# Performance work log

Hardware: AMD Instinct MI355X
Metric: run time of the kernel (lower is better)

Reference implementation:

```python
import jax, jax.numpy as jnp
import numpy as np
from jax import lax

S = 3000      # number of stocks (and number of targets)
F = 6         # raw features
N = 128       # hidden size
L = 40        # lookback length
L_MAX = 10    # max lag
K = 5         # topk leaders


def setup_inputs() -> dict:
    key = jax.random.key(0)
    ks = jax.random.split(key, 16)
    sc = 1.0 / np.sqrt(N)
    u = lambda k, shp, s=sc: jax.random.uniform(k, shp, jnp.float32, -s, s)
    return {
        "X_scaled": jax.random.normal(ks[0], (1, S, L, F), jnp.float32),
        "X_raw": jax.random.normal(ks[1], (1, S, L, F), jnp.float32),
        "target_idx": jax.random.randint(ks[2], (S,), 0, S, jnp.int32),
        "lstm_Wih": u(ks[3], (4 * N, F)),
        "lstm_Whh": u(ks[4], (4 * N, N)),
        "lstm_bih": u(ks[5], (4 * N,)),
        "lstm_bhh": u(ks[6], (4 * N,)),
        "ln_g": jnp.ones((N,), jnp.float32),
        "ln_b": jnp.zeros((N,), jnp.float32),
        "WQ": u(ks[7], (N, N)),
        "WK": u(ks[8], (N, N)),
        "log_temp": jnp.asarray(np.log(N ** 0.25), jnp.float32),
        "lag_bias": jnp.zeros((L_MAX,), jnp.float32),
        "W1": u(ks[9], (64, 2 * F), 1.0 / np.sqrt(2 * F)),
        "b1": jnp.zeros((64,), jnp.float32),
        "W2": u(ks[10], (32, 64), 1.0 / 8.0),
        "b2": jnp.zeros((32,), jnp.float32),
        "W3": u(ks[11], (1, 32), 1.0 / np.sqrt(32)),
        "b3": jnp.zeros((1,), jnp.float32),
    }


def _lstm(x, Wih, Whh, bih, bhh):
    # x: [BS, L, F] -> hidden sequence [BS, L, N]; torch gate order i,f,g,o
    BS = x.shape[0]
    h0 = jnp.zeros((BS, N), x.dtype)
    bias = bih + bhh

    def step(carry, xt):
        h, c = carry
        g = xt @ Wih.T + h @ Whh.T + bias
        i, f, gg, o = jnp.split(g, 4, axis=-1)
        c = jax.nn.sigmoid(f) * c + jax.nn.sigmoid(i) * jnp.tanh(gg)
        h = jax.nn.sigmoid(o) * jnp.tanh(c)
        return (h, c), h

    _, hs = lax.scan(step, (h0, h0), jnp.swapaxes(x, 0, 1))
    return jnp.swapaxes(hs, 0, 1)


def _ln(x, g, b):
    m = x.mean(-1, keepdims=True)
    v = ((x - m) ** 2).mean(-1, keepdims=True)
    return (x - m) / jnp.sqrt(v + 1e-5) * g + b


def _l2norm(x):
    return x / jnp.clip(jnp.linalg.norm(x, axis=-1, keepdims=True), 1e-12)


def reference(X_scaled, X_raw, target_idx, lstm_Wih, lstm_Whh, lstm_bih,
              lstm_bhh, ln_g, ln_b, WQ, WK, log_temp, lag_bias,
              W1, b1, W2, b2, W3, b3):
    # TemporalEncoder: LSTM over B*S sequences + LayerNorm (B=1)
    H = _ln(_lstm(X_scaled.reshape(S, L, F), lstm_Wih, lstm_Whh,
                  lstm_bih, lstm_bhh), ln_g, ln_b)          # [S, L, N]
    X = X_raw[0]                                            # [S, L, F]

    q = _l2norm(H[target_idx, -1] @ WQ.T)                   # [T, N]
    Hk = _l2norm(H[:, L - L_MAX:] @ WK.T)                   # [S, l_max, N]
    temp = jnp.clip(jnp.exp(log_temp), 0.1, N ** 0.5)

    attn = jnp.einsum('tn,sln->tsl', q, Hk) / temp + lag_bias  # [T, S, l_max]
    self_mask = jnp.arange(S)[None, :] == target_idx[:, None]  # [T, S]
    attn = jnp.where(self_mask[:, :, None], -jnp.inf, attn)

    vals, idx = lax.top_k(attn.reshape(-1, S * L_MAX), K)   # [T, K]
    leader = idx // L_MAX
    lag_j = idx % L_MAX
    lag_pos = jnp.clip(L - 1 - (L_MAX - lag_j), 0, L - 1)

    z = X[leader, lag_pos]                                  # [T, K, F]
    w = jax.nn.softmax(vals, axis=1)
    z_agg = (w[..., None] * z).sum(1)                       # [T, F]
    feat = jnp.concatenate([z_agg, z[:, 0]], axis=-1)       # [T, 2F]

    h1 = jax.nn.relu(feat @ W1.T + b1)
    h2 = jax.nn.relu(h1 @ W2.T + b2)
    return (h2 @ W3.T + b3).squeeze(-1)                     # [T]
```

## Files before the change

### kernel.cpp

```cpp
#include <hip/hip_runtime.h>
#include <math.h>

#define S_N 3000
#define NCOLS 30000
#define SCHUNK 8
#define KTILES 938
#define TPC 118
#define PST 17

typedef __bf16 v8bf __attribute__((ext_vector_type(8)));
typedef float v16f __attribute__((ext_vector_type(16)));
typedef float v4f __attribute__((ext_vector_type(4)));

__device__ __forceinline__ float sigm(float x) { return 1.0f / (1.0f + expf(-x)); }

__device__ __forceinline__ bool bet(float av, int ai, float bv, int bi) {
  return (av > bv) || (av == bv && ai < bi);
}

template <int M>
__device__ __forceinline__ void insS(float (&v)[M], int (&ix)[M], float nv, int ni) {
  if (!(nv > v[M - 1])) return;
  bool b[M];
#pragma unroll
  for (int q = 0; q < M; q++) b[q] = nv > v[q];
#pragma unroll
  for (int q = M - 1; q > 0; q--) {
    v[q]  = b[q] ? (b[q - 1] ? v[q - 1] : nv) : v[q];
    ix[q] = b[q] ? (b[q - 1] ? ix[q - 1] : ni) : ix[q];
  }
  if (b[0]) { v[0] = nv; ix[0] = ni; }
}

template <int M>
__device__ __forceinline__ void insF(float (&v)[M], int (&ix)[M], float nv, int ni) {
  if (!bet(nv, ni, v[M - 1], ix[M - 1])) return;
  bool b[M];
#pragma unroll
  for (int q = 0; q < M; q++) b[q] = bet(nv, ni, v[q], ix[q]);
#pragma unroll
  for (int q = M - 1; q > 0; q--) {
    v[q]  = b[q] ? (b[q - 1] ? v[q - 1] : nv) : v[q];
    ix[q] = b[q] ? (b[q - 1] ? ix[q - 1] : ni) : ix[q];
  }
  if (b[0]) { v[0] = nv; ix[0] = ni; }
}

__device__ __forceinline__ unsigned short f2bf_rne(float f) {
  unsigned int u = __float_as_uint(f);
  unsigned int r = (u + 0x7fffu + ((u >> 16) & 1u)) >> 16;
  return (unsigned short)r;
}
__device__ __forceinline__ float bf2f(unsigned short h) {
  return __uint_as_float(((unsigned int)h) << 16);
}

__global__ __launch_bounds__(256) void cvt_wll(
    const float* __restrict__ Whh, unsigned short* __restrict__ Wllf)
{
  int idx = blockIdx.x * 256 + threadIdx.x;
  if (idx >= 128 * 512) return;
  int f = idx >> 9;
  int lane = (idx >> 3) & 63;
  int j = idx & 7;
  int w = f >> 3, tau = (f >> 1) & 3, s = f & 1;
  int kh = w >> 3, g8 = w & 7;
  int gate = g8 * 64 + tau * 16 + (lane & 15);
  int k = kh * 64 + s * 32 + (lane >> 4) * 8 + j;
  float x = Whh[gate * 128 + k];
  unsigned short hi = f2bf_rne(x);
  float r1 = x - bf2f(hi);
  unsigned short lo = f2bf_rne(r1);
  float r2 = r1 - bf2f(lo);
  Wllf[idx] = f2bf_rne(r2);
}

__global__ __launch_bounds__(1024, 4) void lstm_kernel(
    const float* __restrict__ Xs, const float* __restrict__ Wih,
    const float* __restrict__ Whh, const float* __restrict__ bih,
    const float* __restrict__ bhh, const unsigned short* __restrict__ Wllf,
    float* __restrict__ H10)
{
  __shared__ float P[2 * 512 * PST];
  __shared__ __align__(16) __bf16 Asp[3][4][65][8];
  __shared__ float Xb[12 * 240];
  __shared__ float2 WB2[14][128];

  const int tid = threadIdx.x;
  const int s0 = blockIdx.x * 12;
  const int lane = tid & 63;
  const int wv = tid >> 6;
  const int kh = wv >> 3;
  const int g8 = wv & 7;
  const int l15 = lane & 15, lq = lane >> 4;

  for (int i = tid; i < 12 * 240; i += 1024) Xb[i] = Xs[(size_t)s0 * 240 + i];
  for (int i = tid; i < 3 * 4 * 65 * 8; i += 1024)
    ((unsigned short*)Asp)[i] = 0;
  for (int i = tid; i < 14 * 128; i += 1024) {
    int q = i >> 7, n = i & 127;
    float vv[2];
#pragma unroll
    for (int e = 0; e < 2; e++) {
      int r = 2 * q + e;
      if (r < 24) {
        int gate = n + (r / 6) * 128;
        vv[e] = Wih[gate * 6 + r % 6];
      } else {
        int gate = n + (r - 24) * 128;
        vv[e] = bih[gate] + bhh[gate];
      }
    }
    WB2[q][n] = make_float2(vv[0], vv[1]);
  }

  v8bf whi[4][2], wlo[4][2];
#pragma unroll
  for (int tau = 0; tau < 4; tau++)
#pragma unroll
    for (int s = 0; s < 2; s++) {
      int gate = g8 * 64 + tau * 16 + l15;
      int k0 = kh * 64 + s * 32 + lq * 8;
      const float* wp = Whh + gate * 128 + k0;
      v8bf h8, l8;
#pragma unroll
      for (int j = 0; j < 8; j++) {
        float x = wp[j];
        __bf16 bh_ = (__bf16)x;
        float r1 = x - (float)bh_;
        __bf16 bl_ = (__bf16)r1;
        h8[j] = bh_;
        l8[j] = bl_;
      }
      whi[tau][s] = h8;
      wlo[tau][s] = l8;
    }

  const unsigned short* wllbase = Wllf + (size_t)(wv * 8) * 512 + lane * 8;

  float c0 = 0.0f, c1 = 0.0f;
  const int p2n = tid & 127;
  const int p2m = tid >> 7;
  const int rdrow = (lane & 48) | ((lane + 2 * (lane >> 4)) & 15);

  __syncthreads();

#pragma unroll 1
  for (int t = 0; t < 40; t++) {
    v8bf ah[2], al[2], a3[2];
#pragma unroll
    for (int s = 0; s < 2; s++) {
      int ks = kh * 2 + s;
      ah[s] = *(const v8bf*)&Asp[0][ks][rdrow][0];
      al[s] = *(const v8bf*)&Asp[1][ks][rdrow][0];
      a3[s] = *(const v8bf*)&Asp[2][ks][rdrow][0];
    }
#pragma unroll
    for (int tau = 0; tau < 4; tau++) {
      v4f acc = {0.0f, 0.0f, 0.0f, 0.0f};
#pragma unroll
      for (int s = 0; s < 2; s++) {
        v8bf wll = *(const v8bf*)(wllbase + (tau * 2 + s) * 512);
        acc = __builtin_amdgcn_mfma_f32_16x16x32_bf16(ah[s], whi[tau][s], acc, 0, 0, 0);
        acc = __builtin_amdgcn_mfma_f32_16x16x32_bf16(ah[s], wlo[tau][s], acc, 0, 0, 0);
        acc = __builtin_amdgcn_mfma_f32_16x16x32_bf16(al[s], whi[tau][s], acc, 0, 0, 0);
        acc = __builtin_amdgcn_mfma_f32_16x16x32_bf16(al[s], wlo[tau][s], acc, 0, 0, 0);
        acc = __builtin_amdgcn_mfma_f32_16x16x32_bf16(ah[s], wll, acc, 0, 0, 0);
        acc = __builtin_amdgcn_mfma_f32_16x16x32_bf16(a3[s], whi[tau][s], acc, 0, 0, 0);
      }
      if (lq < 3) {
        int gate = g8 * 64 + tau * 16 + l15;
        float* pp = P + kh * (512 * PST) + gate * PST + lq * 4;
#pragma unroll
        for (int reg = 0; reg < 4; reg++) pp[reg] = acc[reg];
      }
    }
    __syncthreads();

#pragma unroll
    for (int task = 0; task < 2; task++) {
      if (task == 1 && tid >= 512) break;
      const int m = task == 0 ? p2m : 8 + p2m;
      const int n = p2n;
      float wb[28];
#pragma unroll
      for (int q = 0; q < 14; q++) {
        float2 v = WB2[q][n];
        wb[2 * q] = v.x;
        wb[2 * q + 1] = v.y;
      }
      const float* xm = Xb + m * 240 + t * 6;
      float xv[6];
#pragma unroll
      for (int f = 0; f < 6; f++) xv[f] = xm[f];
      float g4[4];
#pragma unroll
      for (int g = 0; g < 4; g++) {
        float a = wb[24 + g];
#pragma unroll
        for (int f = 0; f < 6; f++) a = fmaf(wb[g * 6 + f], xv[f], a);
        int gate = n + g * 128;
        a += P[gate * PST + m] + P[512 * PST + gate * PST + m];
        g4[g] = a;
      }
      float& c = task == 0 ? c0 : c1;
      c = sigm(g4[1]) * c + sigm(g4[0]) * tanhf(g4[2]);
      float h = sigm(g4[3]) * tanhf(c);
      if (t >= 30) H10[((size_t)(s0 + m) * 10 + (t - 30)) * 128 + n] = h;
      __bf16 hh = (__bf16)h;
      float r1 = h - (float)hh;
      __bf16 hl = (__bf16)r1;
      float r2 = r1 - (float)hl;
      __bf16 h3 = (__bf16)r2;
      int g = (n >> 3) & 3;
      int ks = n >> 5;
      int j = n & 7;
      int row = 16 * g + ((m + 2 * g) & 15);
      Asp[0][ks][row][j] = hh;
      Asp[1][ks][row][j] = hl;
      Asp[2][ks][row][j] = h3;
    }
    __syncthreads();
  }
}

__global__ __launch_bounds__(256) void proj_kernel(
    const float* __restrict__ In, const float* __restrict__ WK,
    const float* __restrict__ WQ, const float* __restrict__ lng,
    const float* __restrict__ lnb, float* __restrict__ Kn,
    float* __restrict__ Qn, unsigned short* __restrict__ Qhi,
    unsigned short* __restrict__ Qlo)
{
  __shared__ float A_s[16 * 128];
  const int tid = threadIdx.x;
  const int bk = blockIdx.x;
  const bool isQ = bk >= 1875;
  const int inOff = isQ ? 9 * 128 : 0;
  const int inStride = isQ ? 1280 : 128;
  const int nr = isQ ? 3000 : 30000;
  const float* W = isQ ? WQ : WK;
  float* Out = isQ ? Qn : Kn;
  unsigned short* OutHi = isQ ? Qhi : nullptr;
  unsigned short* OutLo = isQ ? Qlo : nullptr;
  const int r0 = (isQ ? bk - 1875 : bk) * 16;

  for (int i = tid; i < 16 * 32; i += 256) {
    int row = i >> 5, c = i & 31;
    int gr = r0 + row;
    float4 v = make_float4(0.f, 0.f, 0.f, 0.f);
    if (gr < nr)
      v = *(const float4*)(In + (size_t)inOff + (size_t)gr * inStride + c * 4);
    *(float4*)(A_s + row * 128 + c * 4) = v;
  }
  __syncthreads();

  {
    const int wvv = tid >> 6, lane = tid & 63;
    const float g0 = lng[lane], g1 = lng[lane + 64];
    const float bb0 = lnb[lane], bb1 = lnb[lane + 64];
#pragma unroll
    for (int p = 0; p < 4; p++) {
      float* hr = A_s + (wvv * 4 + p) * 128;
      float x0 = hr[lane], x1 = hr[lane + 64];
      float s = x0 + x1;
      for (int off = 32; off > 0; off >>= 1) s += __shfl_xor(s, off);
      float mean = s * (1.0f / 128.0f);
      float d0 = x0 - mean, d1 = x1 - mean;
      float v = d0 * d0 + d1 * d1;
      for (int off = 32; off > 0; off >>= 1) v += __shfl_xor(v, off);
      float rstd = 1.0f / sqrtf(v * (1.0f / 128.0f) + 1e-5f);
      hr[lane] = d0 * rstd * g0 + bb0;
      hr[lane + 64] = d1 * rstd * g1 + bb1;
    }
  }
  __syncthreads();

  const int j = tid & 127, rh = tid >> 7;
  const float* wrow = W + j * 128;
  float acc[8] = {0, 0, 0, 0, 0, 0, 0, 0};
  for (int kc = 0; kc < 32; kc++) {
    float4 wv4 = *(const float4*)(wrow + kc * 4);
#pragma unroll
    for (int i = 0; i < 8; i++) {
      float4 a4 = *(const float4*)(A_s + (rh * 8 + i) * 128 + kc * 4);
      acc[i] = fmaf(wv4.x, a4.x, acc[i]);
      acc[i] = fmaf(wv4.y, a4.y, acc[i]);
      acc[i] = fmaf(wv4.z, a4.z, acc[i]);
      acc[i] = fmaf(wv4.w, a4.w, acc[i]);
    }
  }
  __syncthreads();
#pragma unroll
  for (int i = 0; i < 8; i++) A_s[(rh * 8 + i) * 128 + j] = acc[i];
  __syncthreads();

  const int r = tid >> 4, qq = tid & 15;
  float ss = 0.0f;
#pragma unroll
  for (int i = 0; i < 8; i++) {
    float u = A_s[r * 128 + qq + i * 16];
    ss += u * u;
  }
  for (int off = 8; off > 0; off >>= 1) ss += __shfl_xor(ss, off);
  float scale = 1.0f / fmaxf(sqrtf(ss), 1e-12f);
  int gr = r0 + r;
  if (gr < nr) {
#pragma unroll
    for (int i = 0; i < 8; i++) {
      float val = A_s[r * 128 + qq + i * 16] * scale;
      int col = qq + i * 16;
      Out[(size_t)gr * 128 + col] = val;
      if (OutHi) {
        unsigned short h = f2bf_rne(val);
        unsigned short l = f2bf_rne(val - bf2f(h));
        OutHi[(size_t)gr * 128 + col] = h;
        OutLo[(size_t)gr * 128 + col] = l;
      }
    }
  }
}

__global__ __launch_bounds__(256) void cvt_blockK(
    const float* __restrict__ Kn, unsigned short* __restrict__ hi,
    unsigned short* __restrict__ lo)
{
  const int tile = blockIdx.x;
  const int tid = threadIdx.x;
#pragma unroll
  for (int jj = 0; jj < 4; jj++) {
    int i = tid + jj * 256;
    int r = i >> 5;
    int c0 = (i & 31) * 4;
    int row = tile * 32 + r;
    if (row >= NCOLS) continue;
    float4 f = *(const float4*)(Kn + (size_t)row * 128 + c0);
    ushort4 h, l;
    h.x = f2bf_rne(f.x); l.x = f2bf_rne(f.x - bf2f(h.x));
    h.y = f2bf_rne(f.y); l.y = f2bf_rne(f.y - bf2f(h.y));
    h.z = f2bf_rne(f.z); l.z = f2bf_rne(f.z - bf2f(h.z));
    h.w = f2bf_rne(f.w); l.w = f2bf_rne(f.w - bf2f(h.w));
    int s = c0 >> 4, half = (c0 >> 3) & 1, e = c0 & 7;
    size_t idx = (size_t)tile * 4096 + s * 512 + half * 256 + r * 8 + e;
    *(ushort4*)(hi + idx) = h;
    *(ushort4*)(lo + idx) = l;
  }
}

__global__ __launch_bounds__(256, 3) void score_mfma(
    const unsigned short* __restrict__ Qh, const unsigned short* __restrict__ Ql,
    const unsigned short* __restrict__ Kh, const unsigned short* __restrict__ Kl,
    const int* __restrict__ tix, const float* __restrict__ log_temp,
    const float* __restrict__ lag_bias, float* __restrict__ part)
{
  __shared__ float lagS2[42];
  __shared__ float M[256 * 16];
  const int tid = threadIdx.x;
  const int wv = tid >> 6, lane = tid & 63;
  const int half = lane >> 5, tcol = lane & 31;

  const int lid = blockIdx.y * 94 + blockIdx.x;
  const int chunk = lid & 7;
  const int T0 = (lid >> 3) * 32;
  const int tstart = chunk * TPC;
  const int tend = (tstart + TPC < KTILES) ? tstart + TPC : KTILES;

  for (int i = tid; i < 42; i += 256) lagS2[i] = lag_bias[i % 10];

  const int tgt = T0 + tcol;
  const int tgtc = tgt < S_N ? tgt : S_N - 1;
  const int myTix = tix[tgtc];
  const int selfLo = myTix * 10;
  const float invtemp =
      1.0f / fminf(fmaxf(expf(log_temp[0]), 0.1f), 11.313708499f);

  v8bf bh[8], bl[8];
  {
    const size_t qo = (size_t)myTix * 128 + half * 8;
#pragma unroll
    for (int s = 0; s < 8; s++) {
      bh[s] = *(const v8bf*)(Qh + qo + s * 16);
      bl[s] = *(const v8bf*)(Ql + qo + s * 16);
    }
  }
#pragma unroll
  for (int s = 0; s < 8; s++) {
    asm volatile("" : "+v"(bh[s]), "+v"(bl[s]));
  }

  float tv[8]; int ti[8];
#pragma unroll
  for (int q = 0; q < 8; q++) { tv[q] = -3e38f; ti[q] = 0x7fffffff; }

  __syncthreads();

  for (int it = 0; it < 30; it++) {
    const int tile = tstart + it * 4 + wv;
    const int tilec = tile < KTILES ? tile : KTILES - 1;
    const size_t ao = (size_t)tilec * 4096 + half * 256 + tcol * 8;

    v16f acc0, acc1;
#pragma unroll
    for (int q = 0; q < 16; q++) { acc0[q] = 0.0f; acc1[q] = 0.0f; }

#pragma unroll
    for (int s = 0; s < 8; s++) {
      v8bf ah = *(const v8bf*)(Kh + ao + s * 512);
      v8bf al = *(const v8bf*)(Kl + ao + s * 512);
      acc0 = __builtin_amdgcn_mfma_f32_32x32x16_bf16(ah, bh[s], acc0, 0, 0, 0);
      acc1 = __builtin_amdgcn_mfma_f32_32x32x16_bf16(ah, bl[s], acc1, 0, 0, 0);
      acc1 = __builtin_amdgcn_mfma_f32_32x32x16_bf16(al, bh[s], acc1, 0, 0, 0);
    }

    const int cb = tile * 32;
    const int m0 = cb % 10;
    const bool act = tile < tend;
#pragma unroll
    for (int reg = 0; reg < 16; reg++) {
      const int row = (reg & 3) + 8 * (reg >> 2) + 4 * half;
      const int col = cb + row;
      float vsc = fmaf(acc0[reg] + acc1[reg], invtemp, lagS2[m0 + row]);
      if (act && col < NCOLS && (unsigned)(col - selfLo) >= 10u)
        insS<8>(tv, ti, vsc, col);
    }
  }

  {
    float* my = M + tid * 16;
#pragma unroll
    for (int q = 0; q < 8; q++) {
      my[2 * q] = tv[q];
      my[2 * q + 1] = __int_as_float(ti[q]);
    }
  }
  __syncthreads();
  if (tid < 32 && T0 + tid < S_N) {
    float v[8]; int ix[8];
#pragma unroll
    for (int q = 0; q < 8; q++) { v[q] = -3e38f; ix[q] = 0x7fffffff; }
    for (int w = 0; w < 8; w++) {
      const float* src = M + (w * 32 + tid) * 16;
#pragma unroll
      for (int q = 0; q < 8; q++)
        insF<8>(v, ix, src[2 * q], __float_as_int(src[2 * q + 1]));
    }
    float* dst = part + ((size_t)(T0 + tid) * SCHUNK + chunk) * 16;
#pragma unroll
    for (int q = 0; q < 8; q++) {
      dst[2 * q] = v[q];
      dst[2 * q + 1] = __int_as_float(ix[q]);
    }
  }
}

__global__ __launch_bounds__(256) void final_kernel(
    const float* __restrict__ part, const float* __restrict__ Qn,
    const float* __restrict__ Kn, const int* __restrict__ tix,
    const float* __restrict__ log_temp, const float* __restrict__ lag_bias,
    const float* __restrict__ Xraw,
    const float* __restrict__ W1, const float* __restrict__ b1,
    const float* __restrict__ W2, const float* __restrict__ b2,
    const float* __restrict__ W3, const float* __restrict__ b3,
    float* __restrict__ out)
{
  __shared__ float W1s[64 * 12];
  __shared__ float W2s[32 * 64];
  __shared__ float b1s[64];
  __shared__ float b2s[32];
  __shared__ float W3s[32];
  const int tid = threadIdx.x;
  for (int i = tid; i < 768; i += 256) W1s[i] = W1[i];
  for (int i = tid; i < 2048; i += 256) W2s[i] = W2[i];
  if (tid < 64) b1s[tid] = b1[tid];
  if (tid < 32) { b2s[tid] = b2[tid]; W3s[tid] = W3[tid]; }
  __syncthreads();

  int t = blockIdx.x * 256 + tid;
  if (t >= S_N) return;

  float av[8]; int ai[8];
#pragma unroll
  for (int q = 0; q < 8; q++) { av[q] = -3e38f; ai[q] = 0x7fffffff; }
  const float* pp = part + (size_t)t * (SCHUNK * 16);
  for (int c = 0; c < SCHUNK * 8; c++)
    insF<8>(av, ai, pp[2 * c], __float_as_int(pp[2 * c + 1]));

  const float invtemp =
      1.0f / fminf(fmaxf(expf(log_temp[0]), 0.1f), 11.313708499f);
  const float* q = Qn + (size_t)tix[t] * 128;
  const float* kr[8];
#pragma unroll
  for (int j = 0; j < 8; j++) kr[j] = Kn + (size_t)ai[j] * 128;
  float d[8] = {0, 0, 0, 0, 0, 0, 0, 0};
  for (int kc = 0; kc < 32; kc++) {
    float4 q4 = ((const float4*)q)[kc];
#pragma unroll
    for (int j = 0; j < 8; j++) {
      float4 k4 = ((const float4*)kr[j])[kc];
      d[j] = fmaf(q4.x, k4.x, d[j]);
      d[j] = fmaf(q4.y, k4.y, d[j]);
      d[j] = fmaf(q4.z, k4.z, d[j]);
      d[j] = fmaf(q4.w, k4.w, d[j]);
    }
  }

  float v[5]; int ix[5];
#pragma unroll
  for (int qq = 0; qq < 5; qq++) { v[qq] = -3e38f; ix[qq] = 0x7fffffff; }
#pragma unroll
  for (int j = 0; j < 8; j++) {
    int c = ai[j];
    int s = c / 10;
    int lag = c - 10 * s;
    float ev = d[j] * invtemp + lag_bias[lag];
    insF<5>(v, ix, ev, c);
  }

  float e1 = expf(v[1] - v[0]), e2 = expf(v[2] - v[0]),
        e3 = expf(v[3] - v[0]), e4 = expf(v[4] - v[0]);
  float rs = 1.0f / (1.0f + e1 + e2 + e3 + e4);
  float w_[5] = {rs, e1 * rs, e2 * rs, e3 * rs, e4 * rs};

  float feat[12];
#pragma unroll
  for (int f = 0; f < 12; f++) feat[f] = 0.0f;
#pragma unroll
  for (int qq = 0; qq < 5; qq++) {
    int iq = ix[qq];
    int s = iq / 10;
    int l = iq - 10 * s;
    int pos = 29 + l;
    const float* zp = Xraw + (size_t)s * 240 + pos * 6;
#pragma unroll
    for (int f = 0; f < 6; f++) {
      float z = zp[f];
      feat[f] += w_[qq] * z;
      if (qq == 0) feat[6 + f] = z;
    }
  }

  float h1[64];
#pragma unroll 4
  for (int o = 0; o < 64; o++) {
    float acc = b1s[o];
    const float* wr = W1s + o * 12;
#pragma unroll
    for (int f = 0; f < 12; f++) acc = fmaf(wr[f], feat[f], acc);
    h1[o] = fmaxf(acc, 0.0f);
  }
  float rr = b3[0];
#pragma unroll 2
  for (int o = 0; o < 32; o++) {
    float acc = b2s[o];
    const float* wr = W2s + o * 64;
#pragma unroll 8
    for (int k = 0; k < 64; k++) acc = fmaf(wr[k], h1[k], acc);
    rr = fmaf(W3s[o], fmaxf(acc, 0.0f), rr);
  }
  out[t] = rr;
}

extern "C" void kernel_launch(void* const* d_in, const int* in_sizes, int n_in,
                              void* d_out, int out_size, void* d_ws,
                              size_t ws_size, hipStream_t stream) {
  const float* Xs   = (const float*)d_in[0];
  const float* Xraw = (const float*)d_in[1];
  const int*   tix  = (const int*)d_in[2];
  const float* Wih  = (const float*)d_in[3];
  const float* Whh  = (const float*)d_in[4];
  const float* bih  = (const float*)d_in[5];
  const float* bhh  = (const float*)d_in[6];
  const float* ln_g = (const float*)d_in[7];
  const float* ln_b = (const float*)d_in[8];
  const float* WQ   = (const float*)d_in[9];
  const float* WK   = (const float*)d_in[10];
  const float* log_temp = (const float*)d_in[11];
  const float* lag_bias = (const float*)d_in[12];
  const float* W1 = (const float*)d_in[13];
  const float* b1 = (const float*)d_in[14];
  const float* W2 = (const float*)d_in[15];
  const float* b2 = (const float*)d_in[16];
  const float* W3 = (const float*)d_in[17];
  const float* b3 = (const float*)d_in[18];
  float* outp = (float*)d_out;

  float* ws = (float*)d_ws;
  float* H10 = ws;
  unsigned short* Khi = (unsigned short*)ws;
  unsigned short* Klo = (unsigned short*)(ws + 1922000);
  float* Kn  = ws + 3850000;
  float* Qn  = ws + 7690000;
  unsigned short* Qhi = (unsigned short*)(ws + 8074000);
  unsigned short* Qlo = (unsigned short*)(ws + 8266000);
  float* part = ws + 8458000;
  unsigned short* Wllf = (unsigned short*)(ws + 9226000);

  cvt_wll<<<256, 256, 0, stream>>>(Whh, Wllf);
  lstm_kernel<<<250, 1024, 0, stream>>>(Xs, Wih, Whh, bih, bhh, Wllf, H10);
  proj_kernel<<<2063, 256, 0, stream>>>(H10, WK, WQ, ln_g, ln_b, Kn, Qn,
                                        Qhi, Qlo);
  cvt_blockK<<<KTILES, 256, 0, stream>>>(Kn, Khi, Klo);
  {
    dim3 grid(94, SCHUNK);
    score_mfma<<<grid, 256, 0, stream>>>(Qhi, Qlo, Khi, Klo, tix, log_temp,
                                         lag_bias, part);
  }
  final_kernel<<<12, 256, 0, stream>>>(part, Qn, Kn, tix, log_temp, lag_bias,
                                       Xraw, W1, b1, W2, b2, W3, b3, outp);
}
```

Measured before the change: 674.1 us.

## Split LSTM into 6-stock blocks of 512 threads with full-K per wave

The LSTM kernel now processes 6 stocks per block with 8 waves instead of 12 stocks with 16 waves, doubling the grid to 500 blocks. Each wave now holds the full K range of the hidden-to-hidden weights in registers and keeps two accumulators, rather than splitting K across two wave groups. Shared-memory P padding shrinks and the input tile is re-laid out as 8-float padded rows. The aim is better occupancy and spreading across CUs for the latency-bound recurrence, at the cost of higher register pressure and more MFMA work per wave, with the 16-row MFMA now only partly filled by 6 stocks.

```diff
diff --git a/kernel.cpp b/kernel.cpp
--- a/kernel.cpp
+++ b/kernel.cpp
@@ -6,7 +6,7 @@
 #define SCHUNK 8
 #define KTILES 938
 #define TPC 118
-#define PST 17
+#define PST7 7
 
 typedef __bf16 v8bf __attribute__((ext_vector_type(8)));
 typedef float v16f __attribute__((ext_vector_type(16)));
@@ -75,29 +75,31 @@
   Wllf[idx] = f2bf_rne(r2);
 }
 
-__global__ __launch_bounds__(1024, 4) void lstm_kernel(
+__global__ __launch_bounds__(512, 4) void lstm_kernel(
     const float* __restrict__ Xs, const float* __restrict__ Wih,
     const float* __restrict__ Whh, const float* __restrict__ bih,
     const float* __restrict__ bhh, const unsigned short* __restrict__ Wllf,
     float* __restrict__ H10)
 {
-  __shared__ float P[2 * 512 * PST];
+  __shared__ float P[2 * 512 * PST7];
   __shared__ __align__(16) __bf16 Asp[3][4][65][8];
-  __shared__ float Xb[12 * 240];
+  __shared__ __align__(16) float Xb8[6 * 41 * 8];
   __shared__ float2 WB2[14][128];
 
   const int tid = threadIdx.x;
-  const int s0 = blockIdx.x * 12;
+  const int s0 = blockIdx.x * 6;
   const int lane = tid & 63;
-  const int wv = tid >> 6;
-  const int kh = wv >> 3;
-  const int g8 = wv & 7;
+  const int g8 = tid >> 6;
   const int l15 = lane & 15, lq = lane >> 4;
 
-  for (int i = tid; i < 12 * 240; i += 1024) Xb[i] = Xs[(size_t)s0 * 240 + i];
-  for (int i = tid; i < 3 * 4 * 65 * 8; i += 1024)
+  for (int i = tid; i < 6 * 40 * 8; i += 512) {
+    int m = i / 320, r = i - m * 320, t = r >> 3, f = r & 7;
+    Xb8[(m * 41 + t) * 8 + f] =
+        (f < 6) ? Xs[(size_t)(s0 + m) * 240 + t * 6 + f] : 0.0f;
+  }
+  for (int i = tid; i < 3 * 4 * 65 * 8; i += 512)
     ((unsigned short*)Asp)[i] = 0;
-  for (int i = tid; i < 14 * 128; i += 1024) {
+  for (int i = tid; i < 14 * 128; i += 512) {
     int q = i >> 7, n = i & 127;
     float vv[2];
 #pragma unroll
@@ -114,13 +116,13 @@
     WB2[q][n] = make_float2(vv[0], vv[1]);
   }
 
-  v8bf whi[4][2], wlo[4][2];
+  v8bf whi[4][4], wlo[4][4];
 #pragma unroll
   for (int tau = 0; tau < 4; tau++)
 #pragma unroll
-    for (int s = 0; s < 2; s++) {
+    for (int s = 0; s < 4; s++) {
       int gate = g8 * 64 + tau * 16 + l15;
-      int k0 = kh * 64 + s * 32 + lq * 8;
+      int k0 = (s >> 1) * 64 + (s & 1) * 32 + lq * 8;
       const float* wp = Whh + gate * 128 + k0;
       v8bf h8, l8;
 #pragma unroll
@@ -136,51 +138,60 @@
       wlo[tau][s] = l8;
     }
 
-  const unsigned short* wllbase = Wllf + (size_t)(wv * 8) * 512 + lane * 8;
+  const unsigned short* wllbase = Wllf + (size_t)g8 * 4096 + lane * 8;
 
   float c0 = 0.0f, c1 = 0.0f;
   const int p2n = tid & 127;
-  const int p2m = tid >> 7;
+  const int mq = tid >> 7;
   const int rdrow = (lane & 48) | ((lane + 2 * (lane >> 4)) & 15);
 
   __syncthreads();
 
 #pragma unroll 1
   for (int t = 0; t < 40; t++) {
-    v8bf ah[2], al[2], a3[2];
-#pragma unroll
-    for (int s = 0; s < 2; s++) {
-      int ks = kh * 2 + s;
-      ah[s] = *(const v8bf*)&Asp[0][ks][rdrow][0];
-      al[s] = *(const v8bf*)&Asp[1][ks][rdrow][0];
-      a3[s] = *(const v8bf*)&Asp[2][ks][rdrow][0];
+    v8bf ah[4], al[4], a3[4];
+#pragma unroll
+    for (int s = 0; s < 4; s++) {
+      ah[s] = *(const v8bf*)&Asp[0][s][rdrow][0];
+      al[s] = *(const v8bf*)&Asp[1][s][rdrow][0];
+      a3[s] = *(const v8bf*)&Asp[2][s][rdrow][0];
     }
 #pragma unroll
     for (int tau = 0; tau < 4; tau++) {
-      v4f acc = {0.0f, 0.0f, 0.0f, 0.0f};
-#pragma unroll
-      for (int s = 0; s < 2; s++) {
-        v8bf wll = *(const v8bf*)(wllbase + (tau * 2 + s) * 512);
+      v4f accL = {0.0f, 0.0f, 0.0f, 0.0f};
+      v4f accH = {0.0f, 0.0f, 0.0f, 0.0f};
+#pragma unroll
+      for (int s = 0; s < 4; s++) {
+        v8bf wll = *(const v8bf*)(wllbase + (s >> 1) * 32768 +
+                                  (tau * 2 + (s & 1)) * 512);
+        v4f acc = (s < 2) ? accL : accH;
         acc = __builtin_amdgcn_mfma_f32_16x16x32_bf16(ah[s], whi[tau][s], acc, 0, 0, 0);
         acc = __builtin_amdgcn_mfma_f32_16x16x32_bf16(ah[s], wlo[tau][s], acc, 0, 0, 0);
         acc = __builtin_amdgcn_mfma_f32_16x16x32_bf16(al[s], whi[tau][s], acc, 0, 0, 0);
         acc = __builtin_amdgcn_mfma_f32_16x16x32_bf16(al[s], wlo[tau][s], acc, 0, 0, 0);
         acc = __builtin_amdgcn_mfma_f32_16x16x32_bf16(ah[s], wll, acc, 0, 0, 0);
         acc = __builtin_amdgcn_mfma_f32_16x16x32_bf16(a3[s], whi[tau][s], acc, 0, 0, 0);
+        if (s < 2) accL = acc; else accH = acc;
       }
-      if (lq < 3) {
-        int gate = g8 * 64 + tau * 16 + l15;
-        float* pp = P + kh * (512 * PST) + gate * PST + lq * 4;
-#pragma unroll
-        for (int reg = 0; reg < 4; reg++) pp[reg] = acc[reg];
+      int gate = g8 * 64 + tau * 16 + l15;
+      if (lq == 0) {
+        float* pl = P + gate * PST7;
+        float* ph = pl + 512 * PST7;
+#pragma unroll
+        for (int reg = 0; reg < 4; reg++) { pl[reg] = accL[reg]; ph[reg] = accH[reg]; }
+      } else if (lq == 1) {
+        float* pl = P + gate * PST7 + 4;
+        float* ph = pl + 512 * PST7;
+#pragma unroll
+        for (int reg = 0; reg < 2; reg++) { pl[reg] = accL[reg]; ph[reg] = accH[reg]; }
       }
     }
     __syncthreads();
 
 #pragma unroll
     for (int task = 0; task < 2; task++) {
-      if (task == 1 && tid >= 512) break;
-      const int m = task == 0 ? p2m : 8 + p2m;
+      if (task == 1 && tid >= 256) break;
+      const int m = task == 0 ? mq : 4 + mq;
       const int n = p2n;
       float wb[28];
 #pragma unroll
@@ -189,7 +200,7 @@
         wb[2 * q] = v.x;
         wb[2 * q + 1] = v.y;
       }
-      const float* xm = Xb + m * 240 + t * 6;
+      const float* xm = Xb8 + (m * 41 + t) * 8;
       float xv[6];
 #pragma unroll
       for (int f = 0; f < 6; f++) xv[f] = xm[f];
@@ -200,7 +211,7 @@
 #pragma unroll
         for (int f = 0; f < 6; f++) a = fmaf(wb[g * 6 + f], xv[f], a);
         int gate = n + g * 128;
-        a += P[gate * PST + m] + P[512 * PST + gate * PST + m];
+        a += P[gate * PST7 + m] + P[512 * PST7 + gate * PST7 + m];
         g4[g] = a;
       }
       float& c = task == 0 ? c0 : c1;
@@ -595,7 +606,7 @@
   unsigned short* Wllf = (unsigned short*)(ws + 9226000);
 
   cvt_wll<<<256, 256, 0, stream>>>(Whh, Wllf);
-  lstm_kernel<<<250, 1024, 0, stream>>>(Xs, Wih, Whh, bih, bhh, Wllf, H10);
+  lstm_kernel<<<500, 512, 0, stream>>>(Xs, Wih, Whh, bih, bhh, Wllf, H10);
   proj_kernel<<<2063, 256, 0, stream>>>(H10, WK, WQ, ln_g, ln_b, Kn, Qn,
                                         Qhi, Qlo);
   cvt_blockK<<<KTILES, 256, 0, stream>>>(Kn, Khi, Klo);
```

New measurement: 1.296 ms. +92.3%, slower.
